# Performance work log

Measured on AMD Instinct MI355X. Metric: run time of the kernel, lower is better.

Reference implementation:

```python
import jax, jax.numpy as jnp
import numpy as np

NUM_SAMPLES = 5      # samples per line (line_matcher_cfg)
MIN_DIST_PTS = 8.0   # min pixel spacing between samples
TOP_K = 10           # top-k candidate lines for NW matching
GRID_SIZE = 4        # desc map stride
GAP = 0.1            # NW gap penalty


def sample_line_points(line_seg):
    # line_seg: (N, 2, 2) ij endpoints -> pts (N, S, 2), valid (N, S)
    start, end = line_seg[:, 0], line_seg[:, 1]
    lengths = jnp.linalg.norm(end - start, axis=1)
    nsamp = jnp.clip(jnp.floor(lengths / MIN_DIST_PTS), 2.0, float(NUM_SAMPLES))
    k = jnp.arange(NUM_SAMPLES, dtype=line_seg.dtype)
    interval = (end - start) / (nsamp - 1.0)[:, None]          # (N, 2)
    pts = start[:, None, :] + k[None, :, None] * interval[:, None, :]
    valid = k[None, :] < nsamp[:, None]
    pts = jnp.where(valid[..., None], pts, 0.0)                # torch pads with 0
    return pts, valid


def sample_descriptors(desc, pts):
    # Faithful F.grid_sample(bilinear, zeros padding, align_corners=False) after
    # kornia normalize_pixel_coordinates ((size-1) normalization), then L2-norm.
    # desc: (1, D, H, W); pts: (P, 2) ij coords in full-res image.
    D, H, W = desc.shape[1], desc.shape[2], desc.shape[3]
    img_h, img_w = H * GRID_SIZE, W * GRID_SIZE
    xn = 2.0 * pts[:, 1] / (img_w - 1) - 1.0
    yn = 2.0 * pts[:, 0] / (img_h - 1) - 1.0
    ix = ((xn + 1.0) * W - 1.0) / 2.0   # align_corners=False unnormalize
    iy = ((yn + 1.0) * H - 1.0) / 2.0
    x0f = jnp.floor(ix); y0f = jnp.floor(iy)
    wx = ix - x0f; wy = iy - y0f
    x0 = x0f.astype(jnp.int32); y0 = y0f.astype(jnp.int32)
    img = desc[0]

    def gather(xi, yi):
        inb = ((xi >= 0) & (xi < W) & (yi >= 0) & (yi < H)).astype(img.dtype)
        xc = jnp.clip(xi, 0, W - 1); yc = jnp.clip(yi, 0, H - 1)
        return img[:, yc, xc] * inb[None, :]   # (D, P), zeros outside

    v = (gather(x0, y0) * ((1 - wx) * (1 - wy))[None]
         + gather(x0 + 1, y0) * (wx * (1 - wy))[None]
         + gather(x0, y0 + 1) * ((1 - wx) * wy)[None]
         + gather(x0 + 1, y0 + 1) * (wx * wy)[None])
    return v / jnp.linalg.norm(v, axis=0, keepdims=True)


def needleman_wunsch(scores):
    # scores: (B, n, m); sequential DP via nested lax.scan (rows, then cols)
    B, n, m = scores.shape
    s = jnp.transpose(scores, (1, 0, 2)) - GAP  # (n, B, m)

    def row_step(prev_row, srow):               # prev_row (B, m+1), srow (B, m)
        diag = prev_row[:, :-1].T                # (m, B)
        up = prev_row[:, 1:].T                   # (m, B)

        def col_step(left, xs):
            d, u, sc = xs
            cur = jnp.maximum(jnp.maximum(left, u), d + sc)
            return cur, cur

        _, cols = jax.lax.scan(col_step, jnp.zeros((B,), s.dtype), (diag, up, srow.T))
        new_row = jnp.concatenate([jnp.zeros((B, 1), s.dtype), cols.T], axis=1)
        return new_row, None

    final, _ = jax.lax.scan(row_step, jnp.zeros((B, m + 1), s.dtype), s)
    return final[:, -1]


def filter_and_match_lines(scores):
    # scores: (N, M, n, n)
    ls1 = scores.max(3); v1 = (ls1 != -1.0).astype(scores.dtype)
    ls1 = (ls1 * v1).sum(2) / v1.sum(2)
    ls2 = scores.max(2); v2 = (ls2 != -1.0).astype(scores.dtype)
    ls2 = (ls2 * v2).sum(2) / v2.sum(2)
    line_scores = (ls1 + ls2) / 2.0
    topk_lines = jnp.argsort(line_scores, axis=1)[:, -TOP_K:]          # (N, k)
    top = jnp.take_along_axis(scores, topk_lines[:, :, None, None], axis=1)
    top = jnp.concatenate([top, jnp.flip(top, axis=-1)], axis=1)       # (N, 2k, n, n)
    N, top2k, n, m = top.shape
    nw = needleman_wunsch(top.reshape(N * top2k, n, m)).reshape(N, top2k)
    matches = jnp.argmax(nw, axis=1) % (top2k // 2)
    matches = topk_lines[jnp.arange(N), matches]
    return matches, nw


def match_forward(line_seg1, line_seg2, desc1, desc2):
    N, M = line_seg1.shape[0], line_seg2.shape[0]
    pts1, val1 = sample_line_points(line_seg1)
    pts2, val2 = sample_line_points(line_seg2)
    d1 = sample_descriptors(desc1, pts1.reshape(-1, 2))   # (D, N*S)
    d2 = sample_descriptors(desc2, pts2.reshape(-1, 2))   # (D, M*S)
    scores = d1.T @ d2                                    # (N*S, M*S)
    scores = jnp.where(val1.reshape(-1)[:, None], scores, -1.0)
    scores = jnp.where(val2.reshape(-1)[None, :], scores, -1.0)
    scores = scores.reshape(N, NUM_SAMPLES, M, NUM_SAMPLES).transpose(0, 2, 1, 3)
    matches, nw = filter_and_match_lines(scores)
    # cross check
    matches2, _ = filter_and_match_lines(scores.transpose(1, 0, 3, 2))
    mutual = matches2[matches] == jnp.arange(N)
    matches = jnp.where(mutual, matches, -1)
    return matches, nw


def setup_inputs():
    key = jax.random.key(0)
    k1, k2, k3, k4 = jax.random.split(key, 4)
    N = M = 1200; D = 128; H = W = 128
    img = float(H * GRID_SIZE - 1)
    line_seg1 = jax.random.uniform(k1, (N, 2, 2), jnp.float32) * img
    line_seg2 = jax.random.uniform(k2, (M, 2, 2), jnp.float32) * img
    desc1 = jax.random.normal(k3, (1, D, H, W), jnp.float32)
    desc2 = jax.random.normal(k4, (1, D, H, W), jnp.float32)
    return {"line_seg1": line_seg1, "line_seg2": line_seg2, "desc1": desc1, "desc2": desc2}


def reference(line_seg1, line_seg2, desc1, desc2):
    return match_forward(line_seg1, line_seg2, desc1, desc2)
```

## Files before the change

kernel.cpp:

```cpp
#include <hip/hip_runtime.h>
#include <hip/hip_bf16.h>


#define NLINES 1200
#define NS 5
#define DD 128
#define HH 128
#define WW 128
#define HW (HH*WW)
#define IMGM1 511.0f
#define GAPC 0.1f
#define NPAD 1216
#define PPAD (NPAD*NS)
#define KEXT 384
#define NCH (KEXT/32)
#define NGRP (PPAD/16)

typedef __attribute__((ext_vector_type(8))) short short8;
typedef __attribute__((ext_vector_type(4))) float f32x4;

__global__ void transpose_desc(const float* __restrict__ in1, float* __restrict__ out1,
                               const float* __restrict__ in2, float* __restrict__ out2) {
    const float* in = blockIdx.z ? in2 : in1;
    float* out = blockIdx.z ? out2 : out1;
    __shared__ float t[32][33];
    int s0 = blockIdx.x * 32;
    int d0 = blockIdx.y * 32;
    int c = threadIdx.x;
    int r0 = threadIdx.y;
    #pragma unroll
    for (int rr = 0; rr < 32; rr += 8) {
        int d = d0 + r0 + rr;
        t[r0 + rr][c] = in[d * HW + s0 + c];
    }
    __syncthreads();
    #pragma unroll
    for (int rr = 0; rr < 32; rr += 8) {
        int s = s0 + r0 + rr;
        out[s * DD + d0 + c] = t[c][r0 + rr];
    }
}

__global__ void samplepack_kernel(const float* __restrict__ lseg1, const float* __restrict__ lseg2,
                                  const float* __restrict__ tdesc1, const float* __restrict__ tdesc2,
                                  const float* __restrict__ desc1, const float* __restrict__ desc2,
                                  short* __restrict__ Aext, short* __restrict__ Bext,
                                  float* __restrict__ val1, float* __restrict__ val2,
                                  int use_t) {
    int side = blockIdx.y;
    const float* lseg = side ? lseg2 : lseg1;
    const float* tdesc = side ? tdesc2 : tdesc1;
    const float* desc = side ? desc2 : desc1;
    short* Ef = side ? Bext : Aext;
    float* valout = side ? val2 : val1;
    int arole = side ? 0 : 1;

    __shared__ float ds[16][129];
    int g = blockIdx.x;
    int t = threadIdx.x;
    int lane = t & 63, w = t >> 6;

    #pragma unroll
    for (int s = 0; s < 4; ++s) {
        int r = w * 4 + s;
        int pt = g * 16 + r;
        int line = pt / NS;
        int k = pt - line * NS;

        float sy = 0.f, sx = 0.f, ey = 0.f, ex = 0.f;
        if (line < NLINES) {
            sy = lseg[line * 4 + 0]; sx = lseg[line * 4 + 1];
            ey = lseg[line * 4 + 2]; ex = lseg[line * 4 + 3];
        }
        float dy = ey - sy, dx = ex - sx;
        float len = sqrtf(dy * dy + dx * dx);
        float ns = floorf(len * 0.125f);
        ns = fminf(fmaxf(ns, 2.0f), 5.0f);
        float kf = (float)k;
        float validf = (kf < ns) ? 1.0f : 0.0f;
        float py = sy + kf * (dy / (ns - 1.0f));
        float px = sx + kf * (dx / (ns - 1.0f));
        if (validf == 0.0f) { py = 0.0f; px = 0.0f; }

        float xn = 2.0f * px / IMGM1 - 1.0f;
        float yn = 2.0f * py / IMGM1 - 1.0f;
        float ix = ((xn + 1.0f) * (float)WW - 1.0f) * 0.5f;
        float iy = ((yn + 1.0f) * (float)HH - 1.0f) * 0.5f;
        float x0f = floorf(ix), y0f = floorf(iy);
        float wx = ix - x0f, wy = iy - y0f;
        int x0 = (int)x0f, y0 = (int)y0f;

        float w00 = (1.0f - wx) * (1.0f - wy);
        float w10 = wx * (1.0f - wy);
        float w01 = (1.0f - wx) * wy;
        float w11 = wx * wy;

        float v0 = 0.0f, v1 = 0.0f;
        int xs[4] = { x0, x0 + 1, x0,     x0 + 1 };
        int ys[4] = { y0, y0,     y0 + 1, y0 + 1 };
        float ws4[4] = { w00, w10, w01, w11 };
        #pragma unroll
        for (int c = 0; c < 4; ++c) {
            int xi = xs[c], yi = ys[c];
            float inb = (xi >= 0 && xi < WW && yi >= 0 && yi < HH) ? 1.0f : 0.0f;
            int xc = min(max(xi, 0), WW - 1);
            int yc = min(max(yi, 0), HH - 1);
            if (use_t) {
                int base = (yc * WW + xc) * DD;
                v0 += tdesc[base + lane] * inb * ws4[c];
                v1 += tdesc[base + 64 + lane] * inb * ws4[c];
            } else {
                int base = yc * WW + xc;
                v0 += desc[lane * HW + base] * inb * ws4[c];
                v1 += desc[(lane + 64) * HW + base] * inb * ws4[c];
            }
        }
        float ss = v0 * v0 + v1 * v1;
        #pragma unroll
        for (int o = 32; o > 0; o >>= 1) ss += __shfl_xor(ss, o);
        if (ss == 0.0f) ss = 1.0f;
        float nrm = sqrtf(ss);
        ds[r][lane] = v0 / nrm;
        ds[r][64 + lane] = v1 / nrm;
        if (lane == 0) valout[pt] = (line < NLINES) ? validf : 0.0f;
    }
    __syncthreads();

    #pragma unroll
    for (int it = 0; it < 3; ++it) {
        int idx = it * 256 + t;
        int c = idx >> 6, l = idx & 63;
        int q = l >> 4, r = l & 15;
        short8 outv;
        #pragma unroll
        for (int jj = 0; jj < 8; ++jj) {
            int kext = c * 32 + q * 8 + jj;
            int term = kext >> 7, k = kext & 127;
            float x = ds[r][k];
            __hip_bfloat16 h = __float2bfloat16(x);
            short v = *(short*)&h;
            bool lo_term = arole ? (term == 1) : (term == 2);
            if (lo_term) {
                float hf = __bfloat162float(h);
                __hip_bfloat16 lw = __float2bfloat16(x - hf);
                v = *(short*)&lw;
            }
            outv[jj] = v;
        }
        *(short8*)&Ef[((size_t)(g * NCH + c) * 64 + l) * 8] = outv;
    }
}

__launch_bounds__(256, 3)
__global__ void score_kernel(const short* __restrict__ Af, const short* __restrict__ Bf,
                             const float* __restrict__ val1, const float* __restrict__ val2,
                             float* __restrict__ lsc, float* __restrict__ lscT) {
    __shared__ float dump[80 * 161];

    const int t = threadIdx.x;
    const int lane = t & 63;
    const int w = t >> 6;
    const int wm = w >> 1;
    const int wn = w & 1;
    const int gA0 = blockIdx.x * 10;
    const int gB0 = blockIdx.y * 10;

    const short* paw = Af + ((size_t)(gA0 + 5 * wm) * NCH * 64 + lane) * 8;
    const short* pbw = Bf + ((size_t)(gB0 + 5 * wn) * NCH * 64 + lane) * 8;

    f32x4 acc[5][5];
    #pragma unroll
    for (int a = 0; a < 5; ++a)
        #pragma unroll
        for (int b = 0; b < 5; ++b)
            acc[a][b] = (f32x4){0.f, 0.f, 0.f, 0.f};

    #pragma unroll 1
    for (int c = 0; c < NCH; ++c) {
        short8 ca[5], cb[5];
        #pragma unroll
        for (int ti = 0; ti < 5; ++ti) {
            ca[ti] = *(const short8*)(paw + ti * (NCH * 512) + c * 512);
            cb[ti] = *(const short8*)(pbw + ti * (NCH * 512) + c * 512);
        }
        #pragma unroll
        for (int ti = 0; ti < 5; ++ti)
            #pragma unroll
            for (int tj = 0; tj < 5; ++tj)
                acc[ti][tj] = __builtin_amdgcn_mfma_f32_16x16x32_bf16(
                    ca[ti], cb[tj], acc[ti][tj], 0, 0, 0);
    }

    const int i0l = blockIdx.x * 32;
    const int j0l = blockIdx.y * 32;
    #pragma unroll
    for (int p = 0; p < 2; ++p) {
        __syncthreads();
        if (wm == p) {
            #pragma unroll
            for (int ti = 0; ti < 5; ++ti) {
                #pragma unroll
                for (int reg = 0; reg < 4; ++reg) {
                    int rloc = 16 * ti + (lane >> 4) * 4 + reg;
                    #pragma unroll
                    for (int tj = 0; tj < 5; ++tj) {
                        int col = 80 * wn + 16 * tj + (lane & 15);
                        dump[rloc * 161 + col] = acc[ti][tj][reg];
                    }
                }
            }
        }
        __syncthreads();
        #pragma unroll
        for (int e = 0; e < 2; ++e) {
            int q = t * 2 + e;
            int li = q >> 5, lj = q & 31;
            int i = i0l + 16 * p + li;
            int j = j0l + lj;
            if (i < NLINES && j < NLINES) {
                float S[5][5];
                #pragma unroll
                for (int a = 0; a < 5; ++a) {
                    float va = val1[i * NS + a];
                    #pragma unroll
                    for (int b = 0; b < 5; ++b) {
                        float vb = val2[j * NS + b];
                        float sc = dump[(li * 5 + a) * 161 + (lj * 5 + b)];
                        S[a][b] = (va != 0.0f && vb != 0.0f) ? sc : -1.0f;
                    }
                }
                float sum1 = 0.0f, cnt1 = 0.0f;
                #pragma unroll
                for (int a = 0; a < 5; ++a) {
                    float r = S[a][0];
                    #pragma unroll
                    for (int b = 1; b < 5; ++b) r = fmaxf(r, S[a][b]);
                    float v = (r != -1.0f) ? 1.0f : 0.0f;
                    sum1 += r * v; cnt1 += v;
                }
                float sum2 = 0.0f, cnt2 = 0.0f;
                #pragma unroll
                for (int b = 0; b < 5; ++b) {
                    float r = S[0][b];
                    #pragma unroll
                    for (int a = 1; a < 5; ++a) r = fmaxf(r, S[a][b]);
                    float v = (r != -1.0f) ? 1.0f : 0.0f;
                    sum2 += r * v; cnt2 += v;
                }
                lsc[i * NLINES + j] = (sum1 / cnt1 + sum2 / cnt2) * 0.5f;
            }
        }
        #pragma unroll
        for (int e = 0; e < 2; ++e) {
            int q = t * 2 + e;
            int lj = q >> 4, li = q & 15;
            int i = i0l + 16 * p + li;
            int j = j0l + lj;
            if (i < NLINES && j < NLINES) {
                float S[5][5];
                #pragma unroll
                for (int a = 0; a < 5; ++a) {
                    float va = val1[i * NS + a];
                    #pragma unroll
                    for (int b = 0; b < 5; ++b) {
                        float vb = val2[j * NS + b];
                        float sc = dump[(li * 5 + a) * 161 + (lj * 5 + b)];
                        S[a][b] = (va != 0.0f && vb != 0.0f) ? sc : -1.0f;
                    }
                }
                float sum1 = 0.0f, cnt1 = 0.0f;
                #pragma unroll
                for (int a = 0; a < 5; ++a) {
                    float r = S[a][0];
                    #pragma unroll
                    for (int b = 1; b < 5; ++b) r = fmaxf(r, S[a][b]);
                    float v = (r != -1.0f) ? 1.0f : 0.0f;
                    sum1 += r * v; cnt1 += v;
                }
                float sum2 = 0.0f, cnt2 = 0.0f;
                #pragma unroll
                for (int b = 0; b < 5; ++b) {
                    float r = S[0][b];
                    #pragma unroll
                    for (int a = 1; a < 5; ++a) r = fmaxf(r, S[a][b]);
                    float v = (r != -1.0f) ? 1.0f : 0.0f;
                    sum2 += r * v; cnt2 += v;
                }
                lscT[j * NLINES + i] = (sum1 / cnt1 + sum2 / cnt2) * 0.5f;
            }
        }
    }
}

__global__ void topk_kernel(const float* __restrict__ lsc, const float* __restrict__ lscT,
                            int* __restrict__ topk1, int* __restrict__ topk2) {
    __shared__ float wv[4];
    __shared__ int wi[4];
    int rb = blockIdx.x;
    const float* ls = (rb < NLINES) ? (lsc + rb * NLINES) : (lscT + (rb - NLINES) * NLINES);
    int* topk = (rb < NLINES) ? (topk1 + rb * 10) : (topk2 + (rb - NLINES) * 10);
    int t = threadIdx.x;
    int lane = t & 63, w = t >> 6;
    float val[5];
    #pragma unroll
    for (int s = 0; s < 5; ++s) {
        int j = t + 256 * s;
        val[s] = (j < NLINES) ? ls[j] : -1e30f;
    }
    float bv = -1e30f; int bi = -1;
    #pragma unroll
    for (int s = 0; s < 5; ++s) {
        int j = t + 256 * s;
        if (val[s] >= bv) { bv = val[s]; bi = j; }
    }
    for (int sel = 0; sel < 10; ++sel) {
        float rv = bv; int ri = bi;
        #pragma unroll
        for (int o = 32; o > 0; o >>= 1) {
            float ov = __shfl_xor(rv, o);
            int oi = __shfl_xor(ri, o);
            if (ov > rv || (ov == rv && oi > ri)) { rv = ov; ri = oi; }
        }
        if (lane == 0) { wv[w] = rv; wi[w] = ri; }
        __syncthreads();
        float fv = wv[0]; int fi = wi[0];
        #pragma unroll
        for (int qq = 1; qq < 4; ++qq)
            if (wv[qq] > fv || (wv[qq] == fv && wi[qq] > fi)) { fv = wv[qq]; fi = wi[qq]; }
        if (t == 0) topk[9 - sel] = fi;
        if ((fi & 255) == t) {
            val[fi >> 8] = -1e30f;
            bv = -1e30f; bi = -1;
            #pragma unroll
            for (int s = 0; s < 5; ++s) {
                int j = t + 256 * s;
                if (val[s] >= bv) { bv = val[s]; bi = j; }
            }
        }
        __syncthreads();
    }
}

__device__ __forceinline__ float nw5(const float* M) {
    float F[6] = {0, 0, 0, 0, 0, 0};
    #pragma unroll
    for (int x = 0; x < 5; ++x) {
        float diag = F[0];
        float left = 0.0f;
        #pragma unroll
        for (int y = 1; y <= 5; ++y) {
            float up = F[y];
            float cur = fmaxf(fmaxf(left, up), diag + (M[x * 5 + y - 1] - GAPC));
            F[y] = cur; left = cur; diag = up;
        }
    }
    return F[5];
}

__global__ void nw_kernel(const short* __restrict__ Af, const short* __restrict__ Bf,
                          const float* __restrict__ val1, const float* __restrict__ val2,
                          const int* __restrict__ topk1, const int* __restrict__ topk2,
                          float* __restrict__ nwout, float* __restrict__ nw2buf) {
    __shared__ float sbuf[4][25];
    int w4 = threadIdx.x >> 6;
    int gw = blockIdx.x * 4 + w4;
    int lane = threadIdx.x & 63;
    int dir = (gw >= 12000) ? 1 : 0;
    int rem = gw - dir * 12000;
    int row = rem / 10, r = rem - row * 10;
    int i, j;
    if (!dir) { i = row; j = topk1[row * 10 + r]; }
    else      { j = row; i = topk2[row * 10 + r]; }

    int q = lane >> 4, rr = lane & 15;
    int ptA = i * 5 + rr, ptB = j * 5 + rr;
    const short* baseA = Af + ((size_t)((ptA >> 4) * NCH) * 64 + q * 16 + (ptA & 15)) * 8;
    const short* baseB = Bf + ((size_t)((ptB >> 4) * NCH) * 64 + q * 16 + (ptB & 15)) * 8;
    f32x4 acc = (f32x4){0.f, 0.f, 0.f, 0.f};
    #pragma unroll
    for (int c = 0; c < NCH; ++c) {
        short8 a = *(const short8*)(baseA + c * 512);
        short8 b = *(const short8*)(baseB + c * 512);
        acc = __builtin_amdgcn_mfma_f32_16x16x32_bf16(a, b, acc, 0, 0, 0);
    }
    if (lane < 5) {
        #pragma unroll
        for (int reg = 0; reg < 4; ++reg) sbuf[w4][reg * 5 + lane] = acc[reg];
    }
    if (lane >= 16 && lane < 21) sbuf[w4][20 + (lane - 16)] = acc[0];
    __syncthreads();
    if (lane == 0) {
        float S[25];
        #pragma unroll
        for (int a = 0; a < 5; ++a) {
            float va = val1[i * NS + a];
            #pragma unroll
            for (int b = 0; b < 5; ++b) {
                float vb = val2[j * NS + b];
                S[a * 5 + b] = (va != 0.0f && vb != 0.0f) ? sbuf[w4][a * 5 + b] : -1.0f;
            }
        }
        float M1[25], M2[25];
        if (!dir) {
            #pragma unroll
            for (int x = 0; x < 5; ++x)
                #pragma unroll
                for (int y = 0; y < 5; ++y) {
                    M1[x * 5 + y] = S[x * 5 + y];
                    M2[x * 5 + y] = S[x * 5 + (4 - y)];
                }
        } else {
            #pragma unroll
            for (int x = 0; x < 5; ++x)
                #pragma unroll
                for (int y = 0; y < 5; ++y) {
                    M1[x * 5 + y] = S[y * 5 + x];
                    M2[x * 5 + y] = S[(4 - y) * 5 + x];
                }
        }
        float n1 = nw5(M1);
        float n2 = nw5(M2);
        if (!dir) { nwout[row * 20 + r] = n1; nwout[row * 20 + 10 + r] = n2; }
        else      { nw2buf[row * 20 + r] = n1; nw2buf[row * 20 + 10 + r] = n2; }
    }
}

__global__ void argmax_final_kernel(const float* __restrict__ nw1, const float* __restrict__ nw2,
                                    const int* __restrict__ topk1, const int* __restrict__ topk2,
                                    float* __restrict__ out) {
    __shared__ int mpre[NLINES];
    __shared__ int m2[NLINES];
    int t = threadIdx.x;
    for (int qq = t; qq < 2 * NLINES; qq += 1024) {
        int dir = qq / NLINES, row = qq - dir * NLINES;
        const float* nw = (dir ? nw2 : nw1) + row * 20;
        float best = nw[0]; int bi = 0;
        #pragma unroll
        for (int q = 1; q < 20; ++q) {
            float v = nw[q];
            if (v > best) { best = v; bi = q; }
        }
        int m = (dir ? topk2 : topk1)[row * 10 + (bi % 10)];
        if (dir) m2[row] = m; else mpre[row] = m;
    }
    __syncthreads();
    for (int i = t; i < NLINES; i += 1024) {
        int m = mpre[i];
        out[i] = (m2[m] == i) ? (float)m : -1.0f;
    }
}

extern "C" void kernel_launch(void* const* d_in, const int* in_sizes, int n_in,
                              void* d_out, int out_size, void* d_ws, size_t ws_size,
                              hipStream_t stream) {
    const float* lseg1 = (const float*)d_in[0];
    const float* lseg2 = (const float*)d_in[1];
    const float* desc1 = (const float*)d_in[2];
    const float* desc2 = (const float*)d_in[3];
    float* out = (float*)d_out;

    float* wsf = (float*)d_ws;
    size_t off = 0;
    float* val1 = wsf + off;   off += PPAD;
    float* val2 = wsf + off;   off += PPAD;
    float* lsc = wsf + off;    off += (size_t)NLINES * NLINES;
    float* lscT = wsf + off;   off += (size_t)NLINES * NLINES;
    int* topk1 = (int*)(wsf + off); off += NLINES * 10;
    int* topk2 = (int*)(wsf + off); off += NLINES * 10;
    float* nw2buf = wsf + off; off += NLINES * 20;
    short* Aext = (short*)(wsf + off); off += (size_t)PPAD * KEXT / 2;
    short* Bext = (short*)(wsf + off); off += (size_t)PPAD * KEXT / 2;
    float* tdesc1 = wsf + off; off += (size_t)HW * DD;
    float* tdesc2 = wsf + off; off += (size_t)HW * DD;
    size_t need_full = off * sizeof(float);
    int use_t = (ws_size >= need_full) ? 1 : 0;

    if (use_t) {
        transpose_desc<<<dim3(HW / 32, DD / 32, 2), dim3(32, 8), 0, stream>>>(
            desc1, tdesc1, desc2, tdesc2);
    }
    samplepack_kernel<<<dim3(NGRP, 2), 256, 0, stream>>>(
        lseg1, lseg2, tdesc1, tdesc2, desc1, desc2, Aext, Bext, val1, val2, use_t);

    score_kernel<<<dim3(NPAD / 32, NPAD / 32), 256, 0, stream>>>(Aext, Bext, val1, val2,
                                                                 lsc, lscT);

    topk_kernel<<<2 * NLINES, 256, 0, stream>>>(lsc, lscT, topk1, topk2);

    nw_kernel<<<6000, 256, 0, stream>>>(Aext, Bext, val1, val2, topk1, topk2,
                                        out + NLINES, nw2buf);

    argmax_final_kernel<<<1, 1024, 0, stream>>>(out + NLINES, nw2buf, topk1, topk2, out);
}
```

Before: 203.2 us.

## Prefetch score tiles with register double-buffering and batch NW per row

The score kernel now keeps per-tile pointers, fully unrolls the K-chunk loop and loads the next chunk into a second register set while MFMAs run on the current one. Its launch bound drops to 2 blocks per SIMD to leave room for the extra registers. The NW kernel now runs one 64-lane block per line: it loads that line's descriptor fragments once and reuses them across all 10 top-k candidates, packing two candidates into each 16x16 MFMA. The forward and reversed DP are spread over 20 lanes instead of running serially on one lane. The cost is higher register pressure and lower occupancy in both kernels.

```diff
diff --git a/kernel.cpp b/kernel.cpp
--- a/kernel.cpp
+++ b/kernel.cpp
@@ -151,7 +151,7 @@
     }
 }
 
-__launch_bounds__(256, 3)
+__launch_bounds__(256, 2)
 __global__ void score_kernel(const short* __restrict__ Af, const short* __restrict__ Bf,
                              const float* __restrict__ val1, const float* __restrict__ val2,
                              float* __restrict__ lsc, float* __restrict__ lscT) {
@@ -165,8 +165,13 @@
     const int gA0 = blockIdx.x * 10;
     const int gB0 = blockIdx.y * 10;
 
-    const short* paw = Af + ((size_t)(gA0 + 5 * wm) * NCH * 64 + lane) * 8;
-    const short* pbw = Bf + ((size_t)(gB0 + 5 * wn) * NCH * 64 + lane) * 8;
+    const short* pa[5];
+    const short* pb[5];
+    #pragma unroll
+    for (int ti = 0; ti < 5; ++ti) {
+        pa[ti] = Af + ((size_t)(gA0 + 5 * wm + ti) * NCH * 64 + lane) * 8;
+        pb[ti] = Bf + ((size_t)(gB0 + 5 * wn + ti) * NCH * 64 + lane) * 8;
+    }
 
     f32x4 acc[5][5];
     #pragma unroll
@@ -175,13 +180,18 @@
         for (int b = 0; b < 5; ++b)
             acc[a][b] = (f32x4){0.f, 0.f, 0.f, 0.f};
 
-    #pragma unroll 1
-    for (int c = 0; c < NCH; ++c) {
-        short8 ca[5], cb[5];
+    short8 ca[5], cb[5], na[5], nb[5];
+    #pragma unroll
+    for (int ti = 0; ti < 5; ++ti) {
+        ca[ti] = *(const short8*)(pa[ti]);
+        cb[ti] = *(const short8*)(pb[ti]);
+    }
+    #pragma unroll
+    for (int c = 0; c < NCH; c += 2) {
         #pragma unroll
         for (int ti = 0; ti < 5; ++ti) {
-            ca[ti] = *(const short8*)(paw + ti * (NCH * 512) + c * 512);
-            cb[ti] = *(const short8*)(pbw + ti * (NCH * 512) + c * 512);
+            na[ti] = *(const short8*)(pa[ti] + (c + 1) * 512);
+            nb[ti] = *(const short8*)(pb[ti] + (c + 1) * 512);
         }
         #pragma unroll
         for (int ti = 0; ti < 5; ++ti)
@@ -189,6 +199,19 @@
             for (int tj = 0; tj < 5; ++tj)
                 acc[ti][tj] = __builtin_amdgcn_mfma_f32_16x16x32_bf16(
                     ca[ti], cb[tj], acc[ti][tj], 0, 0, 0);
+        if (c + 2 < NCH) {
+            #pragma unroll
+            for (int ti = 0; ti < 5; ++ti) {
+                ca[ti] = *(const short8*)(pa[ti] + (c + 2) * 512);
+                cb[ti] = *(const short8*)(pb[ti] + (c + 2) * 512);
+            }
+        }
+        #pragma unroll
+        for (int ti = 0; ti < 5; ++ti)
+            #pragma unroll
+            for (int tj = 0; tj < 5; ++tj)
+                acc[ti][tj] = __builtin_amdgcn_mfma_f32_16x16x32_bf16(
+                    na[ti], nb[tj], acc[ti][tj], 0, 0, 0);
     }
 
     const int i0l = blockIdx.x * 32;
@@ -361,35 +384,56 @@
                           const float* __restrict__ val1, const float* __restrict__ val2,
                           const int* __restrict__ topk1, const int* __restrict__ topk2,
                           float* __restrict__ nwout, float* __restrict__ nw2buf) {
-    __shared__ float sbuf[4][25];
-    int w4 = threadIdx.x >> 6;
-    int gw = blockIdx.x * 4 + w4;
-    int lane = threadIdx.x & 63;
-    int dir = (gw >= 12000) ? 1 : 0;
-    int rem = gw - dir * 12000;
-    int row = rem / 10, r = rem - row * 10;
-    int i, j;
-    if (!dir) { i = row; j = topk1[row * 10 + r]; }
-    else      { j = row; i = topk2[row * 10 + r]; }
-
+    __shared__ float sbuf[10][25];
+    __shared__ int jl[10];
+    int rb = blockIdx.x;
+    int dir = (rb >= NLINES) ? 1 : 0;
+    int row = rb - dir * NLINES;
+    int lane = threadIdx.x;
     int q = lane >> 4, rr = lane & 15;
-    int ptA = i * 5 + rr, ptB = j * 5 + rr;
-    const short* baseA = Af + ((size_t)((ptA >> 4) * NCH) * 64 + q * 16 + (ptA & 15)) * 8;
-    const short* baseB = Bf + ((size_t)((ptB >> 4) * NCH) * 64 + q * 16 + (ptB & 15)) * 8;
-    f32x4 acc = (f32x4){0.f, 0.f, 0.f, 0.f};
-    #pragma unroll
-    for (int c = 0; c < NCH; ++c) {
-        short8 a = *(const short8*)(baseA + c * 512);
-        short8 b = *(const short8*)(baseB + c * 512);
-        acc = __builtin_amdgcn_mfma_f32_16x16x32_bf16(a, b, acc, 0, 0, 0);
-    }
-    if (lane < 5) {
-        #pragma unroll
-        for (int reg = 0; reg < 4; ++reg) sbuf[w4][reg * 5 + lane] = acc[reg];
-    }
-    if (lane >= 16 && lane < 21) sbuf[w4][20 + (lane - 16)] = acc[0];
+
+    if (lane < 10) jl[lane] = (dir ? topk2 : topk1)[row * 10 + lane];
     __syncthreads();
-    if (lane == 0) {
+
+    const short* shEf = dir ? Bf : Af;
+    const short* cdEf = dir ? Af : Bf;
+
+    int ptS = row * 5 + min(rr, 4);
+    const short* shp = shEf + ((size_t)(ptS >> 4) * NCH * 64 + q * 16 + (ptS & 15)) * 8;
+    short8 sh[NCH];
+    #pragma unroll
+    for (int c = 0; c < NCH; ++c) sh[c] = *(const short8*)(shp + c * 512);
+
+    #pragma unroll
+    for (int pp = 0; pp < 5; ++pp) {
+        int c1 = jl[2 * pp], c2 = jl[2 * pp + 1];
+        int ptC = (rr < 8) ? (c1 * 5 + min(rr, 4)) : (c2 * 5 + min(rr - 8, 4));
+        const short* cp = cdEf + ((size_t)(ptC >> 4) * NCH * 64 + q * 16 + (ptC & 15)) * 8;
+        f32x4 acc = (f32x4){0.f, 0.f, 0.f, 0.f};
+        #pragma unroll
+        for (int c = 0; c < NCH; ++c) {
+            short8 cb = *(const short8*)(cp + c * 512);
+            acc = dir ? __builtin_amdgcn_mfma_f32_16x16x32_bf16(cb, sh[c], acc, 0, 0, 0)
+                      : __builtin_amdgcn_mfma_f32_16x16x32_bf16(sh[c], cb, acc, 0, 0, 0);
+        }
+        #pragma unroll
+        for (int reg = 0; reg < 4; ++reg) {
+            int m = q * 4 + reg, n = rr;
+            if (!dir) {
+                if (m < 5 && n < 5) sbuf[2 * pp][m * 5 + n] = acc[reg];
+                if (m < 5 && n >= 8 && n < 13) sbuf[2 * pp + 1][m * 5 + (n - 8)] = acc[reg];
+            } else {
+                if (m < 5 && n < 5) sbuf[2 * pp][m * 5 + n] = acc[reg];
+                if (m >= 8 && m < 13 && n < 5) sbuf[2 * pp + 1][(m - 8) * 5 + n] = acc[reg];
+            }
+        }
+    }
+    __syncthreads();
+
+    if (lane < 20) {
+        int r = lane >> 1, rev = lane & 1;
+        int i = dir ? jl[r] : row;
+        int j = dir ? row : jl[r];
         float S[25];
         #pragma unroll
         for (int a = 0; a < 5; ++a) {
@@ -397,31 +441,20 @@
             #pragma unroll
             for (int b = 0; b < 5; ++b) {
                 float vb = val2[j * NS + b];
-                S[a * 5 + b] = (va != 0.0f && vb != 0.0f) ? sbuf[w4][a * 5 + b] : -1.0f;
-            }
-        }
-        float M1[25], M2[25];
-        if (!dir) {
-            #pragma unroll
-            for (int x = 0; x < 5; ++x)
-                #pragma unroll
-                for (int y = 0; y < 5; ++y) {
-                    M1[x * 5 + y] = S[x * 5 + y];
-                    M2[x * 5 + y] = S[x * 5 + (4 - y)];
-                }
-        } else {
-            #pragma unroll
-            for (int x = 0; x < 5; ++x)
-                #pragma unroll
-                for (int y = 0; y < 5; ++y) {
-                    M1[x * 5 + y] = S[y * 5 + x];
-                    M2[x * 5 + y] = S[(4 - y) * 5 + x];
-                }
-        }
-        float n1 = nw5(M1);
-        float n2 = nw5(M2);
-        if (!dir) { nwout[row * 20 + r] = n1; nwout[row * 20 + 10 + r] = n2; }
-        else      { nw2buf[row * 20 + r] = n1; nw2buf[row * 20 + 10 + r] = n2; }
+                S[a * 5 + b] = (va != 0.0f && vb != 0.0f) ? sbuf[r][a * 5 + b] : -1.0f;
+            }
+        }
+        float M[25];
+        #pragma unroll
+        for (int x = 0; x < 5; ++x)
+            #pragma unroll
+            for (int y = 0; y < 5; ++y) {
+                if (!dir) M[x * 5 + y] = rev ? S[x * 5 + (4 - y)] : S[x * 5 + y];
+                else      M[x * 5 + y] = rev ? S[(4 - y) * 5 + x] : S[y * 5 + x];
+            }
+        float nwv = nw5(M);
+        float* o = dir ? nw2buf : nwout;
+        o[row * 20 + rev * 10 + r] = nwv;
     }
 }
 
@@ -487,8 +520,8 @@
 
     topk_kernel<<<2 * NLINES, 256, 0, stream>>>(lsc, lscT, topk1, topk2);
 
-    nw_kernel<<<6000, 256, 0, stream>>>(Aext, Bext, val1, val2, topk1, topk2,
-                                        out + NLINES, nw2buf);
+    nw_kernel<<<2 * NLINES, 64, 0, stream>>>(Aext, Bext, val1, val2, topk1, topk2,
+                                             out + NLINES, nw2buf);
 
     argmax_final_kernel<<<1, 1024, 0, stream>>>(out + NLINES, nw2buf, topk1, topk2, out);
 }
```

After: 197.6 us. -2.8%, faster.
